# Performance work log

Measured on AMD Instinct MI355X. Metric: run time of the kernel, lower is better.

## Reference

```python
import jax, jax.numpy as jnp
import numpy as np

HIDDEN = 64
MLP_HID = 40

def setup_inputs() -> dict:
    key = jax.random.key(0)
    ks = jax.random.split(key, 9)
    B, T, H = 256, 4096, HIDDEN
    s_ih = 1.0 / np.sqrt(H)
    inputs = jax.random.normal(ks[0], (B, T), dtype=jnp.float32)
    W_ih = jax.random.uniform(ks[1], (4 * H, 1), jnp.float32, -s_ih, s_ih)
    W_hh = jax.random.uniform(ks[2], (4 * H, H), jnp.float32, -s_ih, s_ih)
    b_ih = jax.random.uniform(ks[3], (4 * H,), jnp.float32, -s_ih, s_ih)
    b_hh = jax.random.uniform(ks[4], (4 * H,), jnp.float32, -s_ih, s_ih)
    s1 = 1.0 / np.sqrt(H + 1)
    W1 = jax.random.uniform(ks[5], (MLP_HID, H + 1), jnp.float32, -s1, s1)
    b1 = jax.random.uniform(ks[6], (MLP_HID,), jnp.float32, -s1, s1)
    s2 = 1.0 / np.sqrt(MLP_HID)
    W2 = jax.random.uniform(ks[7], (1, MLP_HID), jnp.float32, -s2, s2)
    b2 = jax.random.uniform(ks[8], (1,), jnp.float32, -s2, s2)
    return {"inputs": inputs, "W_ih": W_ih, "W_hh": W_hh, "b_ih": b_ih,
            "b_hh": b_hh, "W1": W1, "b1": b1, "W2": W2, "b2": b2}

def _lstm(inputs, W_ih, W_hh, b_ih, b_hh):
    # inputs: [B, T]; input_size = 1 so x projection is an outer product.
    B, T = inputs.shape
    H = W_hh.shape[1]
    # x_proj: [T, B, 4H] (time-major for scan)
    x_proj = inputs.T[:, :, None] * W_ih[:, 0][None, None, :] + (b_ih + b_hh)

    def step(carry, xp):
        h, c = carry
        gates = xp + h @ W_hh.T  # [B, 4H]
        i, f, g, o = jnp.split(gates, 4, axis=-1)
        i = jax.nn.sigmoid(i)
        f = jax.nn.sigmoid(f)
        g = jnp.tanh(g)
        o = jax.nn.sigmoid(o)
        c = f * c + i * g
        h = o * jnp.tanh(c)
        return (h, c), h

    h0 = jnp.zeros((B, H), inputs.dtype)
    c0 = jnp.zeros((B, H), inputs.dtype)
    (_, _), hs = jax.lax.scan(step, (h0, c0), x_proj)
    return hs.transpose(1, 0, 2)  # [B, T, H]

def reference(inputs, W_ih, W_hh, b_ih, b_hh, W1, b1, W2, b2):
    hiddens = _lstm(inputs, W_ih, W_hh, b_ih, b_hh)          # [B, T, H]
    combined = jnp.concatenate([hiddens, inputs[:, :, None]], axis=2)  # [B, T, H+1]
    z = jax.nn.sigmoid(combined @ W1.T + b1)                  # [B, T, 40]
    y = z @ W2.T + b2                                         # [B, T, 1]
    return y[:, :, 0]
```

## Files before the change

kernel.cpp:

```cpp
#include <hip/hip_runtime.h>

#define HIDDEN  64
#define T_LEN   4096
#define CHUNK   32
#define MLP_HID 40
#define HP      68
#define W1P     68
#define ZP      41

__device__ __forceinline__ float fast_sigmoid(float x) {
    float e = __builtin_amdgcn_exp2f(x * -1.4426950408889634f);
    return __builtin_amdgcn_rcpf(1.0f + e);
}
__device__ __forceinline__ float fast_tanh(float x) {
    float e = __builtin_amdgcn_exp2f(x * 2.8853900817779268f);
    return 1.0f - 2.0f * __builtin_amdgcn_rcpf(1.0f + e);
}

__device__ __forceinline__ float dpp_xor1(float v) {
    return __int_as_float(__builtin_amdgcn_update_dpp(
        0, __float_as_int(v), 0xB1, 0xF, 0xF, true));
}
__device__ __forceinline__ float dpp_xor2(float v) {
    return __int_as_float(__builtin_amdgcn_update_dpp(
        0, __float_as_int(v), 0x4E, 0xF, 0xF, true));
}

__global__ __launch_bounds__(256, 1)
void lstm_mlp_kernel(const float* __restrict__ inputs,
                     const float* __restrict__ W_ih,
                     const float* __restrict__ W_hh,
                     const float* __restrict__ b_ih,
                     const float* __restrict__ b_hh,
                     const float* __restrict__ W1,
                     const float* __restrict__ b1,
                     const float* __restrict__ W2,
                     const float* __restrict__ b2,
                     float* __restrict__ out)
{
    __shared__ __align__(16) float x_lds[T_LEN];
    __shared__ __align__(16) float h_hist[CHUNK * HP];
    __shared__ __align__(16) float w1_lds[MLP_HID * W1P];
    __shared__ float b1_lds[MLP_HID];
    __shared__ float w2_lds[MLP_HID];
    __shared__ float z_lds[CHUNK * ZP];

    const int tid = threadIdx.x;
    const int b   = blockIdx.x;
    const int w   = tid >> 6;
    const int l   = tid & 63;
    const int r   = l >> 2;
    const int q   = l & 3;
    const int u   = 16 * w + r;

    const float4* in4 = (const float4*)(inputs + (size_t)b * T_LEN);
    float4* x4 = (float4*)x_lds;
    #pragma unroll
    for (int rr = 0; rr < 4; ++rr) x4[tid + 256 * rr] = in4[tid + 256 * rr];

    float4 wreg[4][4];
    float wih[4], bias[4];
    #pragma unroll
    for (int j = 0; j < 4; ++j) {
        const int g = j * 64 + u;
        const float4* p = (const float4*)(W_hh + g * HIDDEN + 16 * q);
        #pragma unroll
        for (int m = 0; m < 4; ++m) wreg[j][m] = p[m];
        wih[j]  = W_ih[g];
        bias[j] = b_ih[g] + b_hh[g];
    }
    const float b2v = b2[0];

    for (int p = tid; p < MLP_HID * 65; p += 256) {
        int row = p / 65, col = p - row * 65;
        w1_lds[row * W1P + col] = W1[p];
    }
    if (tid < MLP_HID) { b1_lds[tid] = b1[tid]; w2_lds[tid] = W2[tid]; }
    if (tid < HIDDEN)  h_hist[31 * HP + tid] = 0.0f;
    float c = 0.0f;
    __syncthreads();

    float* outb = out + (size_t)b * T_LEN;
    const float* hrow_rd = h_hist + 31 * HP;

    for (int t = 0; t < T_LEN; ++t) {
        const float4* h4 = (const float4*)(hrow_rd + 16 * q);
        float4 hv0 = h4[0], hv1 = h4[1], hv2 = h4[2], hv3 = h4[3];
        float xv = x_lds[t];

        float acc[4];
        #pragma unroll
        for (int j = 0; j < 4; ++j) {
            float a0 = hv0.x * wreg[j][0].x, a1 = hv0.y * wreg[j][0].y;
            float a2 = hv0.z * wreg[j][0].z, a3 = hv0.w * wreg[j][0].w;
            a0 = fmaf(hv1.x, wreg[j][1].x, a0); a1 = fmaf(hv1.y, wreg[j][1].y, a1);
            a2 = fmaf(hv1.z, wreg[j][1].z, a2); a3 = fmaf(hv1.w, wreg[j][1].w, a3);
            a0 = fmaf(hv2.x, wreg[j][2].x, a0); a1 = fmaf(hv2.y, wreg[j][2].y, a1);
            a2 = fmaf(hv2.z, wreg[j][2].z, a2); a3 = fmaf(hv2.w, wreg[j][2].w, a3);
            a0 = fmaf(hv3.x, wreg[j][3].x, a0); a1 = fmaf(hv3.y, wreg[j][3].y, a1);
            a2 = fmaf(hv3.z, wreg[j][3].z, a2); a3 = fmaf(hv3.w, wreg[j][3].w, a3);
            acc[j] = (a0 + a1) + (a2 + a3);
        }
        #pragma unroll
        for (int j = 0; j < 4; ++j) {
            acc[j] += dpp_xor1(acc[j]);
            acc[j] += dpp_xor2(acc[j]);
        }
        float gi = fast_sigmoid(acc[0] + fmaf(xv, wih[0], bias[0]));
        float gf = fast_sigmoid(acc[1] + fmaf(xv, wih[1], bias[1]));
        float gg = fast_tanh   (acc[2] + fmaf(xv, wih[2], bias[2]));
        float go = fast_sigmoid(acc[3] + fmaf(xv, wih[3], bias[3]));
        c = fmaf(gf, c, gi * gg);
        float hn = go * fast_tanh(c);

        const int rw = t & (CHUNK - 1);
        if (q == 0) h_hist[rw * HP + u] = hn;
        __syncthreads();
        hrow_rd = h_hist + rw * HP;

        if (rw == (CHUNK - 1)) {
            int tbase = t - (CHUNK - 1);
            int tl = tid >> 3, j0 = tid & 7;
            float4 hh[16];
            const float4* hr = (const float4*)(h_hist + tl * HP);
            #pragma unroll
            for (int m = 0; m < 16; ++m) hh[m] = hr[m];
            float xc = x_lds[tbase + tl];
            #pragma unroll
            for (int jj = 0; jj < 5; ++jj) {
                int j = j0 + 8 * jj;
                const float4* w1r = (const float4*)(w1_lds + j * W1P);
                float a0 = b1_lds[j], a1 = 0.f, a2 = 0.f, a3 = 0.f;
                #pragma unroll
                for (int m = 0; m < 16; ++m) {
                    float4 wv = w1r[m];
                    a0 = fmaf(hh[m].x, wv.x, a0);
                    a1 = fmaf(hh[m].y, wv.y, a1);
                    a2 = fmaf(hh[m].z, wv.z, a2);
                    a3 = fmaf(hh[m].w, wv.w, a3);
                }
                float zacc = ((a0 + a1) + (a2 + a3)) + xc * w1_lds[j * W1P + 64];
                z_lds[tl * ZP + j] = fast_sigmoid(zacc);
            }
            __syncthreads();
            if (tid < CHUNK) {
                float y = b2v;
                #pragma unroll
                for (int j = 0; j < MLP_HID; ++j)
                    y = fmaf(w2_lds[j], z_lds[tid * ZP + j], y);
                outb[tbase + tid] = y;
            }
        }
    }
}

extern "C" void kernel_launch(void* const* d_in, const int* in_sizes, int n_in,
                              void* d_out, int out_size, void* d_ws, size_t ws_size,
                              hipStream_t stream) {
    const float* inputs = (const float*)d_in[0];
    const float* W_ih   = (const float*)d_in[1];
    const float* W_hh   = (const float*)d_in[2];
    const float* b_ih   = (const float*)d_in[3];
    const float* b_hh   = (const float*)d_in[4];
    const float* W1     = (const float*)d_in[5];
    const float* b1     = (const float*)d_in[6];
    const float* W2     = (const float*)d_in[7];
    const float* b2     = (const float*)d_in[8];
    float* out = (float*)d_out;

    lstm_mlp_kernel<<<dim3(256), dim3(256), 0, stream>>>(
        inputs, W_ih, W_hh, b_ih, b_hh, W1, b1, W2, b2, out);
}
```

Before: 1.729 ms.

## Distribute gate activations across quad lanes and use packed FMA for recurrence

Each of the four lanes in a quad now evaluates just one gate's activation. It does this with a single exp/rcp using lane-specific constants, then exchanges gate values through DPP shuffles, so the quad no longer computes all four gates redundantly. The per-gate dot products use v_pk_fma_f32 packed FMAs. The time loop is split into chunk-sized inner loops, unrolled by 2, so the MLP branch check leaves the per-step path. These changes shorten the serial critical path per timestep, at the cost of extra DPP and select instructions and a reduction-order change.

```diff
diff --git a/kernel.cpp b/kernel.cpp
--- a/kernel.cpp
+++ b/kernel.cpp
@@ -8,13 +8,17 @@
 #define W1P     68
 #define ZP      41
 
+typedef float v2f __attribute__((ext_vector_type(2)));
+
+__device__ __forceinline__ v2f pk_fma(v2f a, v2f b, v2f c) {
+    v2f d;
+    asm("v_pk_fma_f32 %0, %1, %2, %3" : "=v"(d) : "v"(a), "v"(b), "v"(c));
+    return d;
+}
+
 __device__ __forceinline__ float fast_sigmoid(float x) {
     float e = __builtin_amdgcn_exp2f(x * -1.4426950408889634f);
     return __builtin_amdgcn_rcpf(1.0f + e);
-}
-__device__ __forceinline__ float fast_tanh(float x) {
-    float e = __builtin_amdgcn_exp2f(x * 2.8853900817779268f);
-    return 1.0f - 2.0f * __builtin_amdgcn_rcpf(1.0f + e);
 }
 
 __device__ __forceinline__ float dpp_xor1(float v) {
@@ -52,24 +56,32 @@
     const int r   = l >> 2;
     const int q   = l & 3;
     const int u   = 16 * w + r;
+    const bool q1 = (q & 1) != 0;
+    const bool q2 = (q & 2) != 0;
 
     const float4* in4 = (const float4*)(inputs + (size_t)b * T_LEN);
     float4* x4 = (float4*)x_lds;
     #pragma unroll
     for (int rr = 0; rr < 4; ++rr) x4[tid + 256 * rr] = in4[tid + 256 * rr];
 
-    float4 wreg[4][4];
-    float wih[4], bias[4];
+    v2f wq2[4][8];
     #pragma unroll
     for (int j = 0; j < 4; ++j) {
-        const int g = j * 64 + u;
-        const float4* p = (const float4*)(W_hh + g * HIDDEN + 16 * q);
+        const float4* p = (const float4*)(W_hh + (j * 64 + u) * HIDDEN + 16 * q);
         #pragma unroll
-        for (int m = 0; m < 4; ++m) wreg[j][m] = p[m];
-        wih[j]  = W_ih[g];
-        bias[j] = b_ih[g] + b_hh[g];
+        for (int m = 0; m < 4; ++m) {
+            float4 t = p[m];
+            wq2[j][2 * m]     = (v2f){t.x, t.y};
+            wq2[j][2 * m + 1] = (v2f){t.z, t.w};
+        }
     }
-    const float b2v = b2[0];
+    const int   gown = q * 64 + u;
+    const float wq   = W_ih[gown];
+    const float bq   = b_ih[gown] + b_hh[gown];
+    const float m_c  = (q == 2) ?  2.8853900817779268f : -1.4426950408889634f;
+    const float a_c  = (q == 2) ? -2.0f : 1.0f;
+    const float d_c  = (q == 2) ?  1.0f : 0.0f;
+    const float b2v  = b2[0];
 
     for (int p = tid; p < MLP_HID * 65; p += 256) {
         int row = p / 65, col = p - row * 65;
@@ -81,45 +93,63 @@
     __syncthreads();
 
     float* outb = out + (size_t)b * T_LEN;
-    const float* hrow_rd = h_hist + 31 * HP;
-
-    for (int t = 0; t < T_LEN; ++t) {
-        const float4* h4 = (const float4*)(hrow_rd + 16 * q);
-        float4 hv0 = h4[0], hv1 = h4[1], hv2 = h4[2], hv3 = h4[3];
-        float xv = x_lds[t];
-
-        float acc[4];
-        #pragma unroll
-        for (int j = 0; j < 4; ++j) {
-            float a0 = hv0.x * wreg[j][0].x, a1 = hv0.y * wreg[j][0].y;
-            float a2 = hv0.z * wreg[j][0].z, a3 = hv0.w * wreg[j][0].w;
-            a0 = fmaf(hv1.x, wreg[j][1].x, a0); a1 = fmaf(hv1.y, wreg[j][1].y, a1);
-            a2 = fmaf(hv1.z, wreg[j][1].z, a2); a3 = fmaf(hv1.w, wreg[j][1].w, a3);
-            a0 = fmaf(hv2.x, wreg[j][2].x, a0); a1 = fmaf(hv2.y, wreg[j][2].y, a1);
-            a2 = fmaf(hv2.z, wreg[j][2].z, a2); a3 = fmaf(hv2.w, wreg[j][2].w, a3);
-            a0 = fmaf(hv3.x, wreg[j][3].x, a0); a1 = fmaf(hv3.y, wreg[j][3].y, a1);
-            a2 = fmaf(hv3.z, wreg[j][3].z, a2); a3 = fmaf(hv3.w, wreg[j][3].w, a3);
-            acc[j] = (a0 + a1) + (a2 + a3);
+
+    for (int tc = 0; tc < T_LEN / CHUNK; ++tc) {
+        #pragma unroll 2
+        for (int tt = 0; tt < CHUNK; ++tt) {
+            const int t  = tc * CHUNK + tt;
+            const int rw = tt;
+            const float* hrow = h_hist + ((tt + CHUNK - 1) & (CHUNK - 1)) * HP;
+
+            float xv = x_lds[t];
+            v2f hv[8];
+            const float4* h4 = (const float4*)(hrow + 16 * q);
+            #pragma unroll
+            for (int m = 0; m < 4; ++m) {
+                float4 tv = h4[m];
+                hv[2 * m]     = (v2f){tv.x, tv.y};
+                hv[2 * m + 1] = (v2f){tv.z, tv.w};
+            }
+            float acc[4];
+            #pragma unroll
+            for (int j = 0; j < 4; ++j) {
+                v2f a = {0.f, 0.f}, bb = {0.f, 0.f};
+                #pragma unroll
+                for (int m = 0; m < 4; ++m) {
+                    a  = pk_fma(hv[2 * m],     wq2[j][2 * m],     a);
+                    bb = pk_fma(hv[2 * m + 1], wq2[j][2 * m + 1], bb);
+                }
+                v2f s2 = a + bb;
+                acc[j] = s2.x + s2.y;
+            }
+            #pragma unroll
+            for (int j = 0; j < 4; ++j) acc[j] += dpp_xor1(acc[j]);
+            float t0 = q1 ? acc[1] : acc[0];
+            float t1 = q1 ? acc[3] : acc[2];
+            float s_own  = q2 ? t1 : t0;
+            float s_part = q2 ? t0 : t1;
+            float tot = s_own + dpp_xor2(s_part);
+            float pre = tot + fmaf(xv, wq, bq);
+            float act = fmaf(a_c, __builtin_amdgcn_rcpf(
+                              1.0f + __builtin_amdgcn_exp2f(m_c * pre)), d_c);
+            float recv = dpp_xor2(act);
+            float p  = act * recv;
+            float e0 = q2 ? recv : act;
+            float e  = q1 ? e0 : p;
+            float rr = dpp_xor1(e);
+            float fv = q1 ? e : rr;
+            float ig = q1 ? rr : e;
+            c = fmaf(fv, c, ig);
+            float th = fmaf(-2.0f, __builtin_amdgcn_rcpf(
+                             1.0f + __builtin_amdgcn_exp2f(2.8853900817779268f * c)), 1.0f);
+            float ov = q2 ? act : recv;
+            float hn = ov * th;
+            if (q == 1) h_hist[rw * HP + u] = hn;
+            __syncthreads();
         }
-        #pragma unroll
-        for (int j = 0; j < 4; ++j) {
-            acc[j] += dpp_xor1(acc[j]);
-            acc[j] += dpp_xor2(acc[j]);
-        }
-        float gi = fast_sigmoid(acc[0] + fmaf(xv, wih[0], bias[0]));
-        float gf = fast_sigmoid(acc[1] + fmaf(xv, wih[1], bias[1]));
-        float gg = fast_tanh   (acc[2] + fmaf(xv, wih[2], bias[2]));
-        float go = fast_sigmoid(acc[3] + fmaf(xv, wih[3], bias[3]));
-        c = fmaf(gf, c, gi * gg);
-        float hn = go * fast_tanh(c);
-
-        const int rw = t & (CHUNK - 1);
-        if (q == 0) h_hist[rw * HP + u] = hn;
-        __syncthreads();
-        hrow_rd = h_hist + rw * HP;
-
-        if (rw == (CHUNK - 1)) {
-            int tbase = t - (CHUNK - 1);
+
+        {
+            int tbase = tc * CHUNK;
             int tl = tid >> 3, j0 = tid & 7;
             float4 hh[16];
             const float4* hr = (const float4*)(h_hist + tl * HP);
```

Result: faster. 1.469 ms (-15.0%).
